# Kernel optimization log

Hardware: AMD Instinct MI355X
Metric: run time of the kernel (lower is better)

Reference implementation:

```python
import jax, jax.numpy as jnp
import numpy as np

H = 128

def _gru_layer(x_tbi, h0, w_ih, w_hh, b_ih, b_hh):
    # x_tbi: [T, B, in], h0: [B, H]
    # Precompute input-side gates for all timesteps in one big GEMM.
    xg = jnp.einsum('tbi,gi->tbg', x_tbi, w_ih) + b_ih  # [T, B, 3H]

    def step(h, xg_t):
        hg = h @ w_hh.T + b_hh                      # [B, 3H]
        xr, xz, xn = jnp.split(xg_t, 3, axis=-1)
        hr, hz, hn = jnp.split(hg, 3, axis=-1)
        r = jax.nn.sigmoid(xr + hr)
        z = jax.nn.sigmoid(xz + hz)
        n = jnp.tanh(xn + r * hn)
        h_new = (1.0 - z) * n + z * h
        return h_new, h_new

    hT, ys = jax.lax.scan(step, h0, xg)             # ys: [T, B, H]
    return ys, hT


def setup_inputs() -> dict:
    key = jax.random.key(0)
    ks = jax.random.split(key, 12)
    B, T = 64, 4096
    s0 = 1.0 / np.sqrt(H)  # PyTorch GRU init scale
    return {
        'data':  jax.random.normal(ks[0], (B, T, 1), dtype=jnp.float32),
        'hidden': jnp.zeros((2, B, H), dtype=jnp.float32),
        'w_ih0': jax.random.uniform(ks[1], (3 * H, 1), jnp.float32, -s0, s0),
        'w_hh0': jax.random.uniform(ks[2], (3 * H, H), jnp.float32, -s0, s0),
        'b_ih0': jax.random.uniform(ks[3], (3 * H,), jnp.float32, -s0, s0),
        'b_hh0': jax.random.uniform(ks[4], (3 * H,), jnp.float32, -s0, s0),
        'w_ih1': jax.random.uniform(ks[5], (3 * H, H), jnp.float32, -s0, s0),
        'w_hh1': jax.random.uniform(ks[6], (3 * H, H), jnp.float32, -s0, s0),
        'b_ih1': jax.random.uniform(ks[7], (3 * H,), jnp.float32, -s0, s0),
        'b_hh1': jax.random.uniform(ks[8], (3 * H,), jnp.float32, -s0, s0),
        'fc_w':  jax.random.uniform(ks[9], (1, H), jnp.float32, -s0, s0),
        'fc_b':  jax.random.uniform(ks[10], (1,), jnp.float32, -s0, s0),
    }


def reference(data, hidden, w_ih0, w_hh0, b_ih0, b_hh0,
              w_ih1, w_hh1, b_ih1, b_hh1, fc_w, fc_b):
    # data: [B, T, 1] (batch_first). Work in [T, B, ...] for scan.
    x = jnp.transpose(data, (1, 0, 2))
    y0, h0T = _gru_layer(x, hidden[0], w_ih0, w_hh0, b_ih0, b_hh0)
    y1, h1T = _gru_layer(y0, hidden[1], w_ih1, w_hh1, b_ih1, b_hh1)
    out_gru = jnp.transpose(y1, (1, 0, 2))          # [B, T, H]
    out_hidden = jnp.stack([h0T, h1T], axis=0)      # [2, B, H]
    out_data = jax.nn.relu(out_gru) @ fc_w.T + fc_b  # [B, T, 1]
    return out_data, out_hidden
```

## Files before the change

kernel.cpp:

```cpp
#include <hip/hip_runtime.h>

#define TT 4096
#define BB 64
#define RR 16
#define OUT_HID (BB*TT)
#define SPINMAX 100000

#define SYS_LDU(p)    __hip_atomic_load((p),      __ATOMIC_RELAXED, __HIP_MEMORY_SCOPE_SYSTEM)
#define SYS_STU(p,v)  __hip_atomic_store((p),(v), __ATOMIC_RELAXED, __HIP_MEMORY_SCOPE_SYSTEM)
#define SYS_STF(p,v)  __hip_atomic_store((p),(v), __ATOMIC_RELAXED, __HIP_MEMORY_SCOPE_SYSTEM)

__device__ __forceinline__ float sigm(float x) {
    return __builtin_amdgcn_rcpf(1.0f + __expf(-x));
}
__device__ __forceinline__ float tanhfast(float x) {
    return 1.0f - 2.0f * __builtin_amdgcn_rcpf(1.0f + __expf(2.0f * x));
}

#define WAIT_EQ(p, want, cur, dead)                                           \
    if (!(dead)) {                                                            \
        int k_ = 0;                                                           \
        while ((cur) != (unsigned)(want)) {                                   \
            if (++k_ > SPINMAX) { (dead) = true; break; }                     \
            __builtin_amdgcn_s_sleep(1); (cur) = SYS_LDU(p);                  \
        }                                                                     \
    }

#define FMA4(acc, wv, hv)                                            \
    acc = fmaf((wv).x, (hv).x, acc); acc = fmaf((wv).y, (hv).y, acc); \
    acc = fmaf((wv).z, (hv).z, acc); acc = fmaf((wv).w, (hv).w, acc);

#define X8(M) M(0) M(1) M(2) M(3) M(4) M(5) M(6) M(7)

#define DECLW(i) float4 wA##i, wB##i, wC##i;
#define LDW(i)   wA##i = *(const float4*)(rpA + 16*(i)); \
                 wB##i = *(const float4*)(rpB + 16*(i)); \
                 wC##i = *(const float4*)(rpC + 16*(i));
#define PIN1(vv) { float _t0 = (vv).x, _t1 = (vv).y, _t2 = (vv).z, _t3 = (vv).w; \
    asm volatile("" : "+v"(_t0), "+v"(_t1), "+v"(_t2), "+v"(_t3));              \
    (vv).x = _t0; (vv).y = _t1; (vv).z = _t2; (vv).w = _t3; }
#define PINW(i)  PIN1(wA##i) PIN1(wB##i) PIN1(wC##i)
#define DECLY(i) float4 y##i;
#define GEMV_LDS(i) { float4 hv_ = hb4[4*(i) + c]; \
    FMA4(a0, wA##i, hv_); FMA4(a1, wB##i, hv_); FMA4(a2, wC##i, hv_); }
#define GEMV_Y(i) { FMA4(a0, wA##i, y##i); FMA4(a1, wB##i, y##i); FMA4(a2, wC##i, y##i); }

#define RED3() \
    float A0 = a0 + __shfl_xor(a0, 1); A0 += __shfl_xor(A0, 2); \
    float A1 = a1 + __shfl_xor(a1, 1); A1 += __shfl_xor(A1, 2); \
    float A2 = a2 + __shfl_xor(a2, 1); A2 += __shfl_xor(A2, 2);

__global__
__attribute__((amdgpu_flat_work_group_size(512, 512)))
__attribute__((amdgpu_waves_per_eu(2, 2)))
void gru_pipe(
    const float* __restrict__ data,   const float* __restrict__ hidden,
    const float* __restrict__ w_ih0,  const float* __restrict__ w_hh0,
    const float* __restrict__ b_ih0,  const float* __restrict__ b_hh0,
    const float* __restrict__ w_ih1,  const float* __restrict__ w_hh1,
    const float* __restrict__ b_ih1,  const float* __restrict__ b_hh1,
    const float* __restrict__ fc_w,   const float* __restrict__ fc_b,
    float* __restrict__ out, float* __restrict__ wsf)
{
    const int bid  = blockIdx.x;
    const int role = bid >> 6;
    const int b    = bid & 63;
    const int tid  = threadIdx.x;
    const int u    = tid >> 2;
    const int c    = tid & 3;

    float* y0r = wsf;
    float* xgr = wsf + BB*RR*128;
    unsigned* fl   = (unsigned*)(wsf + BB*RR*128 + BB*RR*384);
    unsigned* yflag = fl + 0*BB*RR + b*RR;
    unsigned* ycons = fl + 1*BB*RR + b*RR;
    unsigned* xflag = fl + 2*BB*RR + b*RR;
    unsigned* xcons = fl + 3*BB*RR + b*RR;

    __shared__ __align__(16) float hs[128];
    __shared__ float xs[TT];

    bool dead = false;

    if (role == 0) {
        X8(DECLW)
        { const float* rpA = w_hh0 + u*128 + 4*c;
          const float* rpB = rpA + 16384; const float* rpC = rpA + 32768;
          X8(LDW) }
        X8(PINW)
        const float br  = b_ih0[u]       + b_hh0[u];
        const float bz  = b_ih0[u + 128] + b_hh0[u + 128];
        const float bin = b_ih0[u + 256];
        const float bhn = b_hh0[u + 256];
        const float wir = w_ih0[u], wiz = w_ih0[u + 128], win = w_ih0[u + 256];

        float hold = hidden[b*128 + u];
        if (tid < 128) hs[tid] = hidden[b*128 + tid];
        { const float* xp = data + (size_t)b*TT;
          for (int i = tid; i < TT; i += 512) xs[i] = xp[i]; }
        __syncthreads();

        const float4* hb4 = (const float4*)hs;
        float* yr = y0r + (size_t)b*RR*128;
        unsigned g = 0;

        for (int t = 0; t < TT; ++t) {
            const int s = t & (RR - 1);
            if (tid == 0 && t >= RR) {
                WAIT_EQ(&ycons[s], t - RR + 1, g, dead)
            }
            const float xv = xs[t];
            float a0 = 0.f, a1 = 0.f, a2 = 0.f;
            X8(GEMV_LDS)
            RED3()
            const float r = sigm(fmaf(xv, wir, A0 + br));
            const float z = sigm(fmaf(xv, wiz, A1 + bz));
            const float n = tanhfast(fmaf(r, A2 + bhn, fmaf(xv, win, bin)));
            const float hnew = fmaf(z, hold - n, n);
            __syncthreads();
            if (c == 0) { hs[u] = hnew; SYS_STF(&yr[s*128 + u], hnew); }
            __syncthreads();
            if (tid == 0) SYS_STU(&yflag[s], (unsigned)(t + 1));
            if (t + 1 >= RR) g = SYS_LDU(&ycons[(t + 1) & (RR - 1)]);
            hold = hnew;
        }
        if (tid < 128) out[OUT_HID + b*128 + tid] = hs[tid];

    } else if (role <= 2) {
        X8(DECLW)
        { const float* rpA = w_ih1 + u*128 + 4*c;
          const float* rpB = rpA + 16384; const float* rpC = rpA + 32768;
          X8(LDW) }
        X8(PINW)
        X8(DECLY)
        const int par = role - 1;
        float* xg = xgr + (size_t)b*RR*384;
        const float* yrd = y0r + (size_t)b*RR*128;

        unsigned fy = SYS_LDU(&yflag[par & (RR - 1)]);
        unsigned fx = 0;

        for (int t = par; t < TT; t += 2) {
            const int s = t & (RR - 1);
            WAIT_EQ(&yflag[s], t + 1, fy, dead)
            if (t >= RR) {
                WAIT_EQ(&xcons[s], t - RR + 1, fx, dead)
            }
            const float4* yb = (const float4*)(yrd + s*128 + 4*c);
            asm volatile(
                "global_load_dwordx4 %0, %8, off sc0 sc1\n\t"
                "global_load_dwordx4 %1, %8, off offset:64 sc0 sc1\n\t"
                "global_load_dwordx4 %2, %8, off offset:128 sc0 sc1\n\t"
                "global_load_dwordx4 %3, %8, off offset:192 sc0 sc1\n\t"
                "global_load_dwordx4 %4, %8, off offset:256 sc0 sc1\n\t"
                "global_load_dwordx4 %5, %8, off offset:320 sc0 sc1\n\t"
                "global_load_dwordx4 %6, %8, off offset:384 sc0 sc1\n\t"
                "global_load_dwordx4 %7, %8, off offset:448 sc0 sc1\n\t"
                "s_waitcnt vmcnt(0)"
                : "=&v"(y0), "=&v"(y1), "=&v"(y2), "=&v"(y3),
                  "=&v"(y4), "=&v"(y5), "=&v"(y6), "=&v"(y7)
                : "v"(yb) : "memory");
            fy = SYS_LDU(&yflag[(t + 2) & (RR - 1)]);
            fx = SYS_LDU(&xcons[(t + 2) & (RR - 1)]);
            float a0 = 0.f, a1 = 0.f, a2 = 0.f;
            X8(GEMV_Y)
            RED3()
            if (c == 0) {
                SYS_STF(&xg[s*384 + u],       A0);
                SYS_STF(&xg[s*384 + 128 + u], A1);
                SYS_STF(&xg[s*384 + 256 + u], A2);
            }
            __syncthreads();
            if (tid == 0) {
                SYS_STU(&xflag[s], (unsigned)(t + 1));
                SYS_STU(&ycons[s], (unsigned)(t + 1));
            }
        }

    } else {
        X8(DECLW)
        { const float* rpA = w_hh1 + u*128 + 4*c;
          const float* rpB = rpA + 16384; const float* rpC = rpA + 32768;
          X8(LDW) }
        X8(PINW)
        const float br  = b_ih1[u]       + b_hh1[u];
        const float bz  = b_ih1[u + 128] + b_hh1[u + 128];
        const float bin = b_ih1[u + 256];
        const float bhn = b_hh1[u + 256];
        float fw0 = 0.f, fw1 = 0.f, fb = 0.f;
        if (tid < 64) { fw0 = fc_w[tid]; fw1 = fc_w[tid + 64]; fb = fc_b[0]; }

        float hold = hidden[8192 + b*128 + u];
        if (tid < 128) hs[tid] = hidden[8192 + b*128 + tid];
        __syncthreads();

        const float4* hb4 = (const float4*)hs;
        const float* xgd = xgr + (size_t)b*RR*384;
        float* outp = out + (size_t)b*TT;
        unsigned f = SYS_LDU(&xflag[0]);

        for (int t = 0; t < TT; ++t) {
            const int s = t & (RR - 1);
            WAIT_EQ(&xflag[s], t + 1, f, dead)
            const float* xgp = xgd + s*384 + u;
            float xr, xz, xn;
            asm volatile(
                "global_load_dword %0, %3, off sc0 sc1\n\t"
                "global_load_dword %1, %3, off offset:512 sc0 sc1\n\t"
                "global_load_dword %2, %3, off offset:1024 sc0 sc1"
                : "=&v"(xr), "=&v"(xz), "=&v"(xn) : "v"(xgp) : "memory");
            if (t + 1 < TT) f = SYS_LDU(&xflag[(t + 1) & (RR - 1)]);
            float fcv = 0.f;
            if (tid < 64 && t >= 1)
                fcv = fmaxf(hs[tid], 0.f)*fw0 + fmaxf(hs[tid + 64], 0.f)*fw1;
            float a0 = 0.f, a1 = 0.f, a2 = 0.f;
            X8(GEMV_LDS)
            RED3()
            asm volatile("s_waitcnt vmcnt(0)" : "+v"(xr), "+v"(xz), "+v"(xn));
            const float r = sigm(xr + A0 + br);
            const float z = sigm(xz + A1 + bz);
            const float n = tanhfast(fmaf(r, A2 + bhn, xn + bin));
            const float hnew = fmaf(z, hold - n, n);
            if (tid < 64 && t >= 1) {
#pragma unroll
                for (int off = 1; off < 64; off <<= 1) fcv += __shfl_xor(fcv, off);
                if (tid == 0) outp[t - 1] = fcv + fb;
            }
            __syncthreads();
            if (c == 0) hs[u] = hnew;
            __syncthreads();
            if (tid == 0) SYS_STU(&xcons[s], (unsigned)(t + 1));
            hold = hnew;
        }
        float fcv = 0.f;
        if (tid < 64) {
            fcv = fmaxf(hs[tid], 0.f)*fw0 + fmaxf(hs[tid + 64], 0.f)*fw1;
#pragma unroll
            for (int off = 1; off < 64; off <<= 1) fcv += __shfl_xor(fcv, off);
            if (tid == 0) outp[TT - 1] = fcv + fb;
        }
        if (tid < 128) out[OUT_HID + 8192 + b*128 + tid] = hs[tid];
    }
}

extern "C" void kernel_launch(void* const* d_in, const int* in_sizes, int n_in,
                              void* d_out, int out_size, void* d_ws, size_t ws_size,
                              hipStream_t stream) {
    (void)in_sizes; (void)n_in; (void)out_size; (void)ws_size;
    gru_pipe<<<256, 512, 0, stream>>>(
        (const float*)d_in[0],  (const float*)d_in[1],
        (const float*)d_in[2],  (const float*)d_in[3],
        (const float*)d_in[4],  (const float*)d_in[5],
        (const float*)d_in[6],  (const float*)d_in[7],
        (const float*)d_in[8],  (const float*)d_in[9],
        (const float*)d_in[10], (const float*)d_in[11],
        (float*)d_out, (float*)d_ws);
}
```

Before: 5.882 ms.

## Split each GEMV across 8 lanes with 1024-thread blocks and prefetch layer-1 inputs

```diff
diff --git a/kernel.cpp b/kernel.cpp
--- a/kernel.cpp
+++ b/kernel.cpp
@@ -30,29 +30,39 @@
     acc = fmaf((wv).x, (hv).x, acc); acc = fmaf((wv).y, (hv).y, acc); \
     acc = fmaf((wv).z, (hv).z, acc); acc = fmaf((wv).w, (hv).w, acc);
 
-#define X8(M) M(0) M(1) M(2) M(3) M(4) M(5) M(6) M(7)
-
-#define DECLW(i) float4 wA##i, wB##i, wC##i;
-#define LDW(i)   wA##i = *(const float4*)(rpA + 16*(i)); \
-                 wB##i = *(const float4*)(rpB + 16*(i)); \
-                 wC##i = *(const float4*)(rpC + 16*(i));
+#define X4(M) M(0) M(1) M(2) M(3)
+
 #define PIN1(vv) { float _t0 = (vv).x, _t1 = (vv).y, _t2 = (vv).z, _t3 = (vv).w; \
     asm volatile("" : "+v"(_t0), "+v"(_t1), "+v"(_t2), "+v"(_t3));              \
     (vv).x = _t0; (vv).y = _t1; (vv).z = _t2; (vv).w = _t3; }
+
+#define DECLW(i) float4 wA##i, wB##i, wC##i;
+#define LDW(i)   wA##i = *(const float4*)(rpA + 32*(i)); \
+                 wB##i = *(const float4*)(rpB + 32*(i)); \
+                 wC##i = *(const float4*)(rpC + 32*(i));
 #define PINW(i)  PIN1(wA##i) PIN1(wB##i) PIN1(wC##i)
-#define DECLY(i) float4 y##i;
-#define GEMV_LDS(i) { float4 hv_ = hb4[4*(i) + c]; \
+#define GEMV_LDS(i) { float4 hv_ = hb4[8*(i) + c]; \
     FMA4(a0, wA##i, hv_); FMA4(a1, wB##i, hv_); FMA4(a2, wC##i, hv_); }
-#define GEMV_Y(i) { FMA4(a0, wA##i, y##i); FMA4(a1, wB##i, y##i); FMA4(a2, wC##i, y##i); }
+#define GEMV_YA(i) { FMA4(a0, wA##i, yA##i); FMA4(a1, wB##i, yA##i); FMA4(a2, wC##i, yA##i); }
+#define GEMV_YB(i) { FMA4(a0, wA##i, yB##i); FMA4(a1, wB##i, yB##i); FMA4(a2, wC##i, yB##i); }
 
 #define RED3() \
-    float A0 = a0 + __shfl_xor(a0, 1); A0 += __shfl_xor(A0, 2); \
-    float A1 = a1 + __shfl_xor(a1, 1); A1 += __shfl_xor(A1, 2); \
-    float A2 = a2 + __shfl_xor(a2, 1); A2 += __shfl_xor(A2, 2);
+    float A0 = a0 + __shfl_xor(a0, 1); A0 += __shfl_xor(A0, 2); A0 += __shfl_xor(A0, 4); \
+    float A1 = a1 + __shfl_xor(a1, 1); A1 += __shfl_xor(A1, 2); A1 += __shfl_xor(A1, 4); \
+    float A2 = a2 + __shfl_xor(a2, 1); A2 += __shfl_xor(A2, 2); A2 += __shfl_xor(A2, 4);
+
+#define LOADY(B0,B1,B2,B3,p) asm volatile(                        \
+    "global_load_dwordx4 %0, %4, off sc0 sc1\n\t"                 \
+    "global_load_dwordx4 %1, %4, off offset:128 sc0 sc1\n\t"      \
+    "global_load_dwordx4 %2, %4, off offset:256 sc0 sc1\n\t"      \
+    "global_load_dwordx4 %3, %4, off offset:384 sc0 sc1"          \
+    : "=&v"(B0), "=&v"(B1), "=&v"(B2), "=&v"(B3) : "v"(p) : "memory");
+#define WAITV  { asm volatile("s_waitcnt vmcnt(0)" ::: "memory"); \
+                 __builtin_amdgcn_sched_barrier(0); }
 
 __global__
-__attribute__((amdgpu_flat_work_group_size(512, 512)))
-__attribute__((amdgpu_waves_per_eu(2, 2)))
+__attribute__((amdgpu_flat_work_group_size(1024, 1024)))
+__attribute__((amdgpu_waves_per_eu(4, 4)))
 void gru_pipe(
     const float* __restrict__ data,   const float* __restrict__ hidden,
     const float* __restrict__ w_ih0,  const float* __restrict__ w_hh0,
@@ -66,8 +76,8 @@
     const int role = bid >> 6;
     const int b    = bid & 63;
     const int tid  = threadIdx.x;
-    const int u    = tid >> 2;
-    const int c    = tid & 3;
+    const int u    = tid >> 3;
+    const int c    = tid & 7;
 
     float* y0r = wsf;
     float* xgr = wsf + BB*RR*128;
@@ -83,11 +93,11 @@
     bool dead = false;
 
     if (role == 0) {
-        X8(DECLW)
+        X4(DECLW)
         { const float* rpA = w_hh0 + u*128 + 4*c;
           const float* rpB = rpA + 16384; const float* rpC = rpA + 32768;
-          X8(LDW) }
-        X8(PINW)
+          X4(LDW) }
+        X4(PINW)
         const float br  = b_ih0[u]       + b_hh0[u];
         const float bz  = b_ih0[u + 128] + b_hh0[u + 128];
         const float bin = b_ih0[u + 256];
@@ -97,7 +107,7 @@
         float hold = hidden[b*128 + u];
         if (tid < 128) hs[tid] = hidden[b*128 + tid];
         { const float* xp = data + (size_t)b*TT;
-          for (int i = tid; i < TT; i += 512) xs[i] = xp[i]; }
+          for (int i = tid; i < TT; i += 1024) xs[i] = xp[i]; }
         __syncthreads();
 
         const float4* hb4 = (const float4*)hs;
@@ -111,7 +121,7 @@
             }
             const float xv = xs[t];
             float a0 = 0.f, a1 = 0.f, a2 = 0.f;
-            X8(GEMV_LDS)
+            X4(GEMV_LDS)
             RED3()
             const float r = sigm(fmaf(xv, wir, A0 + br));
             const float z = sigm(fmaf(xv, wiz, A1 + bz));
@@ -126,63 +136,82 @@
         }
         if (tid < 128) out[OUT_HID + b*128 + tid] = hs[tid];
 
-    } else if (role <= 2) {
-        X8(DECLW)
+    } else if (role == 1) {
+        X4(DECLW)
         { const float* rpA = w_ih1 + u*128 + 4*c;
           const float* rpB = rpA + 16384; const float* rpC = rpA + 32768;
-          X8(LDW) }
-        X8(PINW)
-        X8(DECLY)
-        const int par = role - 1;
+          X4(LDW) }
+        X4(PINW)
+        float4 yA0, yA1, yA2, yA3, yB0, yB1, yB2, yB3;
         float* xg = xgr + (size_t)b*RR*384;
         const float* yrd = y0r + (size_t)b*RR*128;
 
-        unsigned fy = SYS_LDU(&yflag[par & (RR - 1)]);
+        unsigned fy = SYS_LDU(&yflag[0]);
+        WAIT_EQ(&yflag[0], 1, fy, dead)
+        { const float* p = yrd + 4*c; LOADY(yA0, yA1, yA2, yA3, p) }
+        fy = SYS_LDU(&yflag[1]);
         unsigned fx = 0;
 
-        for (int t = par; t < TT; t += 2) {
-            const int s = t & (RR - 1);
-            WAIT_EQ(&yflag[s], t + 1, fy, dead)
-            if (t >= RR) {
-                WAIT_EQ(&xcons[s], t - RR + 1, fx, dead)
-            }
-            const float4* yb = (const float4*)(yrd + s*128 + 4*c);
-            asm volatile(
-                "global_load_dwordx4 %0, %8, off sc0 sc1\n\t"
-                "global_load_dwordx4 %1, %8, off offset:64 sc0 sc1\n\t"
-                "global_load_dwordx4 %2, %8, off offset:128 sc0 sc1\n\t"
-                "global_load_dwordx4 %3, %8, off offset:192 sc0 sc1\n\t"
-                "global_load_dwordx4 %4, %8, off offset:256 sc0 sc1\n\t"
-                "global_load_dwordx4 %5, %8, off offset:320 sc0 sc1\n\t"
-                "global_load_dwordx4 %6, %8, off offset:384 sc0 sc1\n\t"
-                "global_load_dwordx4 %7, %8, off offset:448 sc0 sc1\n\t"
-                "s_waitcnt vmcnt(0)"
-                : "=&v"(y0), "=&v"(y1), "=&v"(y2), "=&v"(y3),
-                  "=&v"(y4), "=&v"(y5), "=&v"(y6), "=&v"(y7)
-                : "v"(yb) : "memory");
-            fy = SYS_LDU(&yflag[(t + 2) & (RR - 1)]);
-            fx = SYS_LDU(&xcons[(t + 2) & (RR - 1)]);
-            float a0 = 0.f, a1 = 0.f, a2 = 0.f;
-            X8(GEMV_Y)
-            RED3()
-            if (c == 0) {
-                SYS_STF(&xg[s*384 + u],       A0);
-                SYS_STF(&xg[s*384 + 128 + u], A1);
-                SYS_STF(&xg[s*384 + 256 + u], A2);
-            }
-            __syncthreads();
-            if (tid == 0) {
-                SYS_STU(&xflag[s], (unsigned)(t + 1));
-                SYS_STU(&ycons[s], (unsigned)(t + 1));
+        for (int t = 0; t < TT; t += 2) {
+            {
+                const int sn = (t + 1) & (RR - 1);
+                WAIT_EQ(&yflag[sn], t + 2, fy, dead)
+                WAITV
+                { const float* p = yrd + sn*128 + 4*c; LOADY(yB0, yB1, yB2, yB3, p) }
+                fy = SYS_LDU(&yflag[(t + 2) & (RR - 1)]);
+                const int s = t & (RR - 1);
+                if (t >= RR) { WAIT_EQ(&xcons[s], t - RR + 1, fx, dead) }
+                fx = SYS_LDU(&xcons[(t + 1) & (RR - 1)]);
+                float a0 = 0.f, a1 = 0.f, a2 = 0.f;
+                X4(GEMV_YA)
+                RED3()
+                if (c == 0) {
+                    SYS_STF(&xg[s*384 + u],       A0);
+                    SYS_STF(&xg[s*384 + 128 + u], A1);
+                    SYS_STF(&xg[s*384 + 256 + u], A2);
+                }
+                __syncthreads();
+                if (tid == 0) {
+                    SYS_STU(&xflag[s], (unsigned)(t + 1));
+                    SYS_STU(&ycons[s], (unsigned)(t + 1));
+                }
+            }
+            {
+                const int tt = t + 1;
+                if (tt + 1 < TT) {
+                    const int sn = (tt + 1) & (RR - 1);
+                    WAIT_EQ(&yflag[sn], tt + 2, fy, dead)
+                    WAITV
+                    { const float* p = yrd + sn*128 + 4*c; LOADY(yA0, yA1, yA2, yA3, p) }
+                    fy = SYS_LDU(&yflag[(tt + 2) & (RR - 1)]);
+                } else {
+                    WAITV
+                }
+                const int s = tt & (RR - 1);
+                if (tt >= RR) { WAIT_EQ(&xcons[s], tt - RR + 1, fx, dead) }
+                fx = SYS_LDU(&xcons[(tt + 1) & (RR - 1)]);
+                float a0 = 0.f, a1 = 0.f, a2 = 0.f;
+                X4(GEMV_YB)
+                RED3()
+                if (c == 0) {
+                    SYS_STF(&xg[s*384 + u],       A0);
+                    SYS_STF(&xg[s*384 + 128 + u], A1);
+                    SYS_STF(&xg[s*384 + 256 + u], A2);
+                }
+                __syncthreads();
+                if (tid == 0) {
+                    SYS_STU(&xflag[s], (unsigned)(tt + 1));
+                    SYS_STU(&ycons[s], (unsigned)(tt + 1));
+                }
             }
         }
 
     } else {
-        X8(DECLW)
+        X4(DECLW)
         { const float* rpA = w_hh1 + u*128 + 4*c;
           const float* rpB = rpA + 16384; const float* rpC = rpA + 32768;
-          X8(LDW) }
-        X8(PINW)
+          X4(LDW) }
+        X4(PINW)
         const float br  = b_ih1[u]       + b_hh1[u];
         const float bz  = b_ih1[u + 128] + b_hh1[u + 128];
         const float bin = b_ih1[u + 256];
@@ -214,9 +243,10 @@
             if (tid < 64 && t >= 1)
                 fcv = fmaxf(hs[tid], 0.f)*fw0 + fmaxf(hs[tid + 64], 0.f)*fw1;
             float a0 = 0.f, a1 = 0.f, a2 = 0.f;
-            X8(GEMV_LDS)
+            X4(GEMV_LDS)
             RED3()
             asm volatile("s_waitcnt vmcnt(0)" : "+v"(xr), "+v"(xz), "+v"(xn));
+            __builtin_amdgcn_sched_barrier(0);
             const float r = sigm(xr + A0 + br);
             const float z = sigm(xz + A1 + bz);
             const float n = tanhfast(fmaf(r, A2 + bhn, xn + bin));
@@ -247,7 +277,7 @@
                               void* d_out, int out_size, void* d_ws, size_t ws_size,
                               hipStream_t stream) {
     (void)in_sizes; (void)n_in; (void)out_size; (void)ws_size;
-    gru_pipe<<<256, 512, 0, stream>>>(
+    gru_pipe<<<192, 1024, 0, stream>>>(
         (const float*)d_in[0],  (const float*)d_in[1],
         (const float*)d_in[2],  (const float*)d_in[3],
         (const float*)d_in[4],  (const float*)d_in[5],
```

Result: slower. 6.382 ms (+8.5%).
